# Kernel optimization log

Hardware: AMD Instinct MI355X
Metric: run time of the kernel (lower is better)

The kernel has to match this reference:

```python
import jax, jax.numpy as jnp
import numpy as np

B, C, S, H, W = 8, 64, 64, 128, 128
HID = 32           # max(C//2, 8)
STEPS, DT, OMEGA_MAX = 10, 0.3, 2.0
EPS = 1e-5


def _dw(x, k):
    # depthwise 3x3 conv, NCHW, kernel [C,1,3,3]
    return jax.lax.conv_general_dilated(
        x, k, (1, 1), 'SAME',
        dimension_numbers=('NCHW', 'OIHW', 'NCHW'),
        feature_group_count=x.shape[1])


def _pw(x, w, b=None):
    # pointwise (1x1) conv as einsum, w: [out,in]
    y = jnp.einsum('bihw,oi->bohw', x, w)
    return y if b is None else y + b[None, :, None, None]


def _lrelu(x):
    return jax.nn.leaky_relu(x, 0.2)


def setup_inputs() -> dict:
    key = jax.random.key(0)
    ks = jax.random.split(key, 16)
    d = {
        'force': jax.random.normal(ks[0], (B, C, H, W), jnp.float32),
        'style': jax.random.normal(ks[1], (1, S, 1, 1), jnp.float32),
        'illum_feat': jax.random.normal(ks[2], (B, C, H, W), jnp.float32),
        # HyperEncoder 1x1 convs
        'h_w1': 0.05 * jax.random.normal(ks[3], (HID, C + S), jnp.float32),
        'h_b1': jnp.zeros((HID,), jnp.float32),
        'h_w2': 0.05 * jax.random.normal(ks[4], (HID, HID), jnp.float32),
        'h_b2': jnp.zeros((HID,), jnp.float32),
        'h_w3': 0.05 * jax.random.normal(ks[5], (4 * C, HID), jnp.float32),
        'h_b3': jnp.zeros((4 * C,), jnp.float32),
        # OscillatorCell convs (no bias)
        'dw_k': 0.05 * jax.random.normal(ks[6], (C, 1, 3, 3), jnp.float32),
        'pw_w': 0.05 * jax.random.normal(ks[7], (C, C), jnp.float32),
        # refine: dw3x3 (+bias), pw, lrelu, pw
        'r_dw_k': 0.05 * jax.random.normal(ks[8], (C, 1, 3, 3), jnp.float32),
        'r_dw_b': jnp.zeros((C,), jnp.float32),
        'r_pw1_w': 0.05 * jax.random.normal(ks[9], (C, C), jnp.float32),
        'r_pw1_b': jnp.zeros((C,), jnp.float32),
        'r_pw2_w': 0.05 * jax.random.normal(ks[10], (C, C), jnp.float32),
        'r_pw2_b': jnp.zeros((C,), jnp.float32),
        'layer_scale': 0.01 * jnp.ones((1, C, 1, 1), jnp.float32),
    }
    return d


def reference(force, style, illum_feat,
              h_w1, h_b1, h_w2, h_b2, h_w3, h_b3,
              dw_k, pw_w,
              r_dw_k, r_dw_b, r_pw1_w, r_pw1_b, r_pw2_w, r_pw2_b,
              layer_scale):
    force = force + 0.2 * illum_feat
    b, c, h, w = force.shape

    # HyperEncoder
    style_map = jnp.broadcast_to(style, (b, style.shape[1], h, w))
    u = jnp.concatenate([force, style_map], axis=1)
    u = _lrelu(_pw(u, h_w1, h_b1))
    u = _lrelu(_pw(u, h_w2, h_b2))
    p = _pw(u, h_w3, h_b3)
    wch, zch, gch, bch = jnp.split(p, 4, axis=1)
    omega = jax.nn.sigmoid(wch) * OMEGA_MAX
    zeta = jax.nn.sigmoid(zch)
    gamma = jax.nn.sigmoid(gch) * 2.0
    beta = jnp.tanh(bch)

    # unrolled symplectic-Euler oscillator recurrence
    def step(carry, _):
        x, v = carry
        coupling = _dw(x, dw_k) + _pw(x, pw_w)
        accel = force + coupling - 2.0 * zeta * omega * v - omega ** 2 * x
        v = v + accel * DT
        x = x + v * DT
        return (x, v), None

    x0 = jnp.zeros_like(force)
    (x, v), _ = jax.lax.scan(step, (x0, x0), None, length=STEPS)

    # instance norm (no affine) + style modulation
    fx = force + x
    mu = fx.mean(axis=(2, 3), keepdims=True)
    var = fx.var(axis=(2, 3), keepdims=True)
    out = gamma * ((fx - mu) / jnp.sqrt(var + EPS)) + beta

    # refine branch with layer scale
    r = _dw(out, r_dw_k) + r_dw_b[None, :, None, None]
    r = _lrelu(_pw(r, r_pw1_w, r_pw1_b))
    r = _pw(r, r_pw2_w, r_pw2_b)
    out = out + layer_scale * r
    return (out, x, v)
```

## Files before the change

### kernel.cpp

```cpp
#include <hip/hip_runtime.h>
#include <hip/hip_fp16.h>

#define Hn 128
#define Wn 128
#define HWn 16384
#define Cn 64
#define Bn 8
#define NTOT (Bn*Cn*HWn)
#define NPIX (Bn*HWn)
#define DTc 0.3f
#define EPSc 1e-5f

__device__ __forceinline__ float sigm(float t){ return 1.0f/(1.0f+__expf(-t)); }

__global__ void fuseF0(const float4* __restrict__ force, const float4* __restrict__ illum,
                       __half* __restrict__ F, __half* __restrict__ XA, __half* __restrict__ V)
{
    int i = blockIdx.x * blockDim.x + threadIdx.x;
    float4 f = force[i], il = illum[i];
    float a0 = f.x + 0.2f*il.x, a1 = f.y + 0.2f*il.y;
    float a2 = f.z + 0.2f*il.z, a3 = f.w + 0.2f*il.w;
    uint2 pf, px, pv;
    __half2 h;
    h = __floats2half2_rn(a0, a1);            pf.x = *(unsigned int*)&h;
    h = __floats2half2_rn(a2, a3);            pf.y = *(unsigned int*)&h;
    h = __floats2half2_rn(0.09f*a0, 0.09f*a1); px.x = *(unsigned int*)&h;
    h = __floats2half2_rn(0.09f*a2, 0.09f*a3); px.y = *(unsigned int*)&h;
    h = __floats2half2_rn(0.3f*a0, 0.3f*a1);   pv.x = *(unsigned int*)&h;
    h = __floats2half2_rn(0.3f*a2, 0.3f*a3);   pv.y = *(unsigned int*)&h;
    *reinterpret_cast<uint2*>(F  + 4*(size_t)i) = pf;
    *reinterpret_cast<uint2*>(XA + 4*(size_t)i) = px;
    *reinterpret_cast<uint2*>(V  + 4*(size_t)i) = pv;
}

__global__ void prep(const float* __restrict__ style, const float* __restrict__ w1,
                     const float* __restrict__ b1, const float* __restrict__ pw,
                     const float* __restrict__ pw1, const float* __restrict__ pw2,
                     const float* __restrict__ w3, const float* __restrict__ b3,
                     float* __restrict__ w1T, float* __restrict__ c1,
                     float* __restrict__ pwT, float* __restrict__ pw1T,
                     float* __restrict__ pw2T,
                     __half2* __restrict__ w3abP, __half2* __restrict__ w3gbP,
                     __half2* __restrict__ b3abP, __half2* __restrict__ b3gbP)
{
    int t = threadIdx.x;
    if (t < 32) {
        float s = b1[t];
        for (int k = 0; k < 64; k++) s += w1[t*128 + 64 + k] * style[k];
        c1[t] = s;
    }
    for (int i = t; i < 2048; i += 256) { int c = i >> 5, j = i & 31; w1T[i] = w1[j*128 + c]; }
    for (int i = t; i < 4096; i += 256) {
        int c = i >> 6, k = i & 63;
        pwT[i]  = pw[k*64 + c];
        pw1T[i] = pw1[k*64 + c];
        pw2T[i] = pw2[k*64 + c];
    }
    for (int i = t; i < 2048; i += 256) {
        int j = i >> 5, k = i & 31;
        w3abP[i] = __floats2half2_rn(w3[j*32 + k],         w3[(64 + j)*32 + k]);
        w3gbP[i] = __floats2half2_rn(w3[(128 + j)*32 + k], w3[(192 + j)*32 + k]);
    }
    if (t < 64) {
        b3abP[t] = __floats2half2_rn(b3[t],       b3[64 + t]);
        b3gbP[t] = __floats2half2_rn(b3[128 + t], b3[192 + t]);
    }
}

__global__ __launch_bounds__(256)
void hyperU(const __half* __restrict__ F,
            const float* __restrict__ w1T, const float* __restrict__ c1,
            const float* __restrict__ w2, const float* __restrict__ b2,
            __half* __restrict__ U2)
{
    __shared__ __half fs[64][256];
    int t = threadIdx.x;
    int p0 = blockIdx.x << 8;
    int b  = p0 >> 14;
    int sp0 = p0 & (HWn - 1);
    int tbase = b * Cn * HWn + sp0;

#pragma unroll
    for (int it = 0; it < 8; it++) {
        int f = t + (it << 8);
        int c = f >> 5, u = f & 31;
        uint4 d = *reinterpret_cast<const uint4*>(F + tbase + c*HWn + (u << 3));
        *reinterpret_cast<uint4*>(&fs[c][u << 3]) = d;
    }
    __syncthreads();

    float u1[32];
#pragma unroll
    for (int j = 0; j < 32; j++) u1[j] = c1[j];
#pragma unroll 4
    for (int c = 0; c < 64; c++) {
        float fc = __half2float(fs[c][t]);
        const float* __restrict__ wr = w1T + c*32;
#pragma unroll
        for (int j = 0; j < 32; j++) u1[j] += wr[j] * fc;
    }
#pragma unroll
    for (int j = 0; j < 32; j++) { float v = u1[j]; u1[j] = v > 0.f ? v : 0.2f*v; }

    float u2[32];
#pragma unroll
    for (int i = 0; i < 32; i++) {
        float s = b2[i];
#pragma unroll
        for (int j = 0; j < 32; j++) s += w2[i*32 + j] * u1[j];
        u2[i] = s > 0.f ? s : 0.2f*s;
    }

    uint4* dst = reinterpret_cast<uint4*>(U2 + ((size_t)(p0 + t)) * 32);
#pragma unroll
    for (int q = 0; q < 4; q++) {
        __half2 h0 = __floats2half2_rn(u2[8*q+0], u2[8*q+1]);
        __half2 h1 = __floats2half2_rn(u2[8*q+2], u2[8*q+3]);
        __half2 h2 = __floats2half2_rn(u2[8*q+4], u2[8*q+5]);
        __half2 h3 = __floats2half2_rn(u2[8*q+6], u2[8*q+7]);
        uint4 d;
        d.x = *(unsigned int*)&h0; d.y = *(unsigned int*)&h1;
        d.z = *(unsigned int*)&h2; d.w = *(unsigned int*)&h3;
        dst[q] = d;
    }
}

__global__ __launch_bounds__(256)
void hyperW(const __half* __restrict__ U2,
            const __half2* __restrict__ w3abP, const __half2* __restrict__ w3gbP,
            const __half2* __restrict__ b3abP, const __half2* __restrict__ b3gbP,
            __half2* __restrict__ AB, __half2* __restrict__ GB)
{
    int p = blockIdx.x * blockDim.x + threadIdx.x;
    int b  = p >> 14;
    int sp = p & (HWn - 1);
    int base = b * Cn * HWn + sp;

    __half2 u2b[32];
    const uint4* src = reinterpret_cast<const uint4*>(U2 + (size_t)p * 32);
#pragma unroll
    for (int q = 0; q < 4; q++) {
        uint4 d = src[q];
        __half2 h;
        h = *(__half2*)&d.x; u2b[8*q+0] = __half2half2(__low2half(h)); u2b[8*q+1] = __half2half2(__high2half(h));
        h = *(__half2*)&d.y; u2b[8*q+2] = __half2half2(__low2half(h)); u2b[8*q+3] = __half2half2(__high2half(h));
        h = *(__half2*)&d.z; u2b[8*q+4] = __half2half2(__low2half(h)); u2b[8*q+5] = __half2half2(__high2half(h));
        h = *(__half2*)&d.w; u2b[8*q+6] = __half2half2(__low2half(h)); u2b[8*q+7] = __half2half2(__high2half(h));
    }

    if (blockIdx.y == 0) {
#pragma unroll 2
        for (int j = 0; j < 64; j++) {
            __half2 aab = b3abP[j];
            const __half2* __restrict__ wa = w3abP + j*32;
#pragma unroll
            for (int i = 0; i < 32; i++) aab = __hfma2(wa[i], u2b[i], aab);
            float2 tab = __half22float2(aab);
            float om = 2.0f * sigm(tab.x);
            float ze = sigm(tab.y);
            AB[base + j*HWn] = __floats2half2_rn(2.0f * ze * om, om * om);
        }
    } else {
#pragma unroll 2
        for (int j = 0; j < 64; j++) {
            __half2 agb = b3gbP[j];
            const __half2* __restrict__ wg = w3gbP + j*32;
#pragma unroll
            for (int i = 0; i < 32; i++) agb = __hfma2(wg[i], u2b[i], agb);
            float2 tgb = __half22float2(agb);
            GB[base + j*HWn] = __floats2half2_rn(2.0f * sigm(tgb.x), tanhf(tgb.y));
        }
    }
}

template <bool LAST>
__global__ void osc_step(const __half* __restrict__ Xin, __half* __restrict__ Xout,
                         __half* __restrict__ V, const __half* __restrict__ F,
                         const __half2* __restrict__ AB,
                         const float* __restrict__ dwk, const float* __restrict__ pwT,
                         float* __restrict__ Xf, float* __restrict__ Vf)
{
    int wid  = blockIdx.x;
    int slot = wid >> 3;
    int pc   = ((wid & 7) << 6) + (slot >> 2);
    int c0   = (slot & 3) << 4;
    int p = (pc << 8) + threadIdx.x;
    int b  = p >> 14;
    int sp = p & (HWn - 1);
    int y = sp >> 7, x = sp & 127;
    int base = b * Cn * HWn + sp;

    float acc[16];
#pragma unroll
    for (int k = 0; k < 16; k++) acc[k] = 0.f;
#pragma unroll 4
    for (int c = 0; c < 64; c++) {
        float xc = __half2float(Xin[base + c*HWn]);
        const float* __restrict__ wr = pwT + c*64 + c0;
#pragma unroll
        for (int k = 0; k < 16; k++) acc[k] += wr[k] * xc;
    }

    int   yo[3] = { y > 0 ? -Wn : 0, 0, y < Hn-1 ? Wn : 0 };
    int   xo[3] = { x > 0 ? -1  : 0, 0, x < Wn-1 ? 1  : 0 };
    float my[3] = { y > 0 ? 1.f : 0.f, 1.f, y < Hn-1 ? 1.f : 0.f };
    float mx[3] = { x > 0 ? 1.f : 0.f, 1.f, x < Wn-1 ? 1.f : 0.f };
    float mm[9]; int oo[9];
#pragma unroll
    for (int dy = 0; dy < 3; dy++)
#pragma unroll
        for (int dx = 0; dx < 3; dx++) { mm[dy*3+dx] = my[dy]*mx[dx]; oo[dy*3+dx] = yo[dy]+xo[dx]; }

#pragma unroll
    for (int cc = 0; cc < 16; cc++) {
        int c = c0 + cc;
        int cb = base + c*HWn;
        float tv[9];
#pragma unroll
        for (int t = 0; t < 9; t++) tv[t] = __half2float(Xin[cb + oo[t]]);
        float dws = 0.f;
#pragma unroll
        for (int t = 0; t < 9; t++) dws += (dwk[c*9 + t] * mm[t]) * tv[t];
        float xc = tv[4];
        float2 ab = __half22float2(AB[cb]);
        float vv = __half2float(V[cb]);
        float accel = __half2float(F[cb]) + acc[cc] + dws - ab.x * vv - ab.y * xc;
        vv += accel * DTc;
        float xn = xc + vv * DTc;
        if constexpr (!LAST) {
            V[cb] = __float2half(vv);
            Xout[cb] = __float2half(xn);
        } else {
            Xf[cb] = xn;
            Vf[cb] = vv;
        }
    }
}

__global__ void inorm_stats(const __half* __restrict__ F, const float* __restrict__ X,
                            float* __restrict__ mu, float* __restrict__ rs)
{
    int bc = blockIdx.x;
    int base = bc * HWn;
    const __half2* __restrict__ F2 = (const __half2*)(F + base);
    const float4*  __restrict__ X4 = (const float4*)(X + base);
    float s = 0.f, s2 = 0.f;
    for (int i = threadIdx.x; i < HWn/4; i += blockDim.x) {
        float4 xv = X4[i];
        float2 f0 = __half22float2(F2[2*i]);
        float2 f1 = __half22float2(F2[2*i+1]);
        float v0 = f0.x + xv.x, v1 = f0.y + xv.y, v2 = f1.x + xv.z, v3 = f1.y + xv.w;
        s += (v0 + v1) + (v2 + v3);
        s2 += (v0*v0 + v1*v1) + (v2*v2 + v3*v3);
    }
#pragma unroll
    for (int o = 32; o > 0; o >>= 1) { s += __shfl_down(s, o); s2 += __shfl_down(s2, o); }
    __shared__ float sh[16];
    int w = threadIdx.x >> 6, l = threadIdx.x & 63;
    if (l == 0) { sh[w] = s; sh[8 + w] = s2; }
    __syncthreads();
    if (threadIdx.x == 0) {
        float S = 0.f, S2 = 0.f;
        for (int i = 0; i < 4; i++) { S += sh[i]; S2 += sh[8 + i]; }
        float m = S / (float)HWn;
        float var = S2 / (float)HWn - m*m;
        mu[bc] = m;
        rs[bc] = rsqrtf(var + EPSc);
    }
}

__global__ void modulate(const __half* __restrict__ F, const float4* __restrict__ X4,
                         const uint4* __restrict__ GBu, const float* __restrict__ mu,
                         const float* __restrict__ rs, __half* __restrict__ outp)
{
    int e4 = blockIdx.x * blockDim.x + threadIdx.x;
    int bc = e4 >> 12;
    float m = mu[bc], r = rs[bc];
    uint2 fu = *reinterpret_cast<const uint2*>(F + 4*(size_t)e4);
    float2 f0 = __half22float2(*(__half2*)&fu.x);
    float2 f1 = __half22float2(*(__half2*)&fu.y);
    float4 xv = X4[e4];
    uint4 gb = GBu[e4];
    float2 g0 = __half22float2(*(__half2*)&gb.x);
    float2 g1 = __half22float2(*(__half2*)&gb.y);
    float2 g2 = __half22float2(*(__half2*)&gb.z);
    float2 g3 = __half22float2(*(__half2*)&gb.w);
    float o0 = g0.x * ((f0.x + xv.x - m) * r) + g0.y;
    float o1 = g1.x * ((f0.y + xv.y - m) * r) + g1.y;
    float o2 = g2.x * ((f1.x + xv.z - m) * r) + g2.y;
    float o3 = g3.x * ((f1.y + xv.w - m) * r) + g3.y;
    __half2 h01 = __floats2half2_rn(o0, o1);
    __half2 h23 = __floats2half2_rn(o2, o3);
    uint2 pack; pack.x = *(unsigned int*)&h01; pack.y = *(unsigned int*)&h23;
    *reinterpret_cast<uint2*>(outp + 4*(size_t)e4) = pack;
}

__global__ __launch_bounds__(512)
void refine(const __half* __restrict__ outp,
            const float* __restrict__ rdwk, const float* __restrict__ rdwb,
            const float* __restrict__ pw1T, const float* __restrict__ pb1,
            const float* __restrict__ pw2T, const float* __restrict__ pb2,
            const float* __restrict__ ls, float* __restrict__ out)
{
    __shared__ unsigned int rv2_s[64][64];
    __shared__ unsigned int act2_s[64][64];
    __shared__ __half w1s[64][64];
    __shared__ __half w2s[64][64];
    __shared__ float  dwks[576];
    __shared__ __half2 pb1h[32], pb2h[32];
    __shared__ float  rdwbs[64], lss[64];
    int t = threadIdx.x;
    for (int i = t; i < 4096; i += 512) {
        w1s[i>>6][i&63] = __float2half(pw1T[i]);
        w2s[i>>6][i&63] = __float2half(pw2T[i]);
    }
    for (int i = t; i < 576; i += 512) dwks[i] = rdwk[i];
    if (t < 64) { rdwbs[t]=rdwb[t]; lss[t]=ls[t]; }
    if (t < 32) {
        pb1h[t] = __floats2half2_rn(pb1[2*t], pb1[2*t+1]);
        pb2h[t] = __floats2half2_rn(pb2[2*t], pb2[2*t+1]);
    }

    int l  = t & 63;
    int g  = t >> 6;
    int c0 = g << 3;
    int row = blockIdx.x;
    int b = row >> 7, y = row & 127;
    int base = b * Cn * HWn + y * Wn;
    int px0 = l << 1;

    int   yo[3] = { y > 0 ? -Wn : 0, 0, y < Hn-1 ? Wn : 0 };
    float my[3] = { y > 0 ? 1.f : 0.f, 1.f, y < Hn-1 ? 1.f : 0.f };
    float wl = l > 0  ? 1.f : 0.f;
    float wr = l < 63 ? 1.f : 0.f;
    int loff = l > 0 ? -1 : 0;
    __syncthreads();

#pragma unroll
    for (int cc = 0; cc < 8; cc++) {
        int c = c0 + cc;
        int cb = base + c*HWn + px0;
        float rv0 = rdwbs[c], rv1 = rdwbs[c];
#pragma unroll
        for (int r = 0; r < 3; r++) {
            const __half* __restrict__ rp = outp + cb + yo[r];
            unsigned int cu = *reinterpret_cast<const unsigned int*>(rp);
            float2 ct = __half22float2(*(__half2*)&cu);
            float lf = __half2float(rp[loff]);
            float rt = __half2float(rp[2]);
            float k0 = dwks[c*9 + r*3 + 0] * my[r];
            float k1 = dwks[c*9 + r*3 + 1] * my[r];
            float k2 = dwks[c*9 + r*3 + 2] * my[r];
            rv0 += k0*(wl*lf) + k1*ct.x + k2*ct.y;
            rv1 += k0*ct.x + k1*ct.y + k2*(wr*rt);
        }
        __half2 hv = __floats2half2_rn(rv0, rv1);
        rv2_s[c][l] = *(unsigned int*)&hv;
    }
    __syncthreads();

    __half2 accA[4], accB[4];
#pragma unroll
    for (int q = 0; q < 4; q++) { accA[q] = pb1h[(c0 >> 1) + q]; accB[q] = accA[q]; }
#pragma unroll 8
    for (int c = 0; c < 64; c++) {
        unsigned int rvu = rv2_s[c][l];
        __half2 rvp = *(__half2*)&rvu;
        __half2 r0 = __half2half2(__low2half(rvp));
        __half2 r1 = __half2half2(__high2half(rvp));
        uint4 wq = *reinterpret_cast<const uint4*>(&w1s[c][c0]);
        __half2 w01 = *(__half2*)&wq.x, w23 = *(__half2*)&wq.y;
        __half2 w45 = *(__half2*)&wq.z, w67 = *(__half2*)&wq.w;
        accA[0] = __hfma2(w01, r0, accA[0]); accB[0] = __hfma2(w01, r1, accB[0]);
        accA[1] = __hfma2(w23, r0, accA[1]); accB[1] = __hfma2(w23, r1, accB[1]);
        accA[2] = __hfma2(w45, r0, accA[2]); accB[2] = __hfma2(w45, r1, accB[2]);
        accA[3] = __hfma2(w67, r0, accA[3]); accB[3] = __hfma2(w67, r1, accB[3]);
    }
#pragma unroll
    for (int q = 0; q < 4; q++) {
        float2 a0 = __half22float2(accA[q]);
        float2 a1 = __half22float2(accB[q]);
        float e0 = a0.x > 0.f ? a0.x : 0.2f*a0.x;
        float e1 = a0.y > 0.f ? a0.y : 0.2f*a0.y;
        float e2 = a1.x > 0.f ? a1.x : 0.2f*a1.x;
        float e3 = a1.y > 0.f ? a1.y : 0.2f*a1.y;
        __half2 p0 = __floats2half2_rn(e0, e2);
        __half2 p1 = __floats2half2_rn(e1, e3);
        act2_s[c0 + 2*q][l]     = *(unsigned int*)&p0;
        act2_s[c0 + 2*q + 1][l] = *(unsigned int*)&p1;
    }
    __syncthreads();

#pragma unroll
    for (int q = 0; q < 4; q++) { accA[q] = pb2h[(c0 >> 1) + q]; accB[q] = accA[q]; }
#pragma unroll 8
    for (int j = 0; j < 64; j++) {
        unsigned int au = act2_s[j][l];
        __half2 ap = *(__half2*)&au;
        __half2 a0 = __half2half2(__low2half(ap));
        __half2 a1 = __half2half2(__high2half(ap));
        uint4 wq = *reinterpret_cast<const uint4*>(&w2s[j][c0]);
        __half2 w01 = *(__half2*)&wq.x, w23 = *(__half2*)&wq.y;
        __half2 w45 = *(__half2*)&wq.z, w67 = *(__half2*)&wq.w;
        accA[0] = __hfma2(w01, a0, accA[0]); accB[0] = __hfma2(w01, a1, accB[0]);
        accA[1] = __hfma2(w23, a0, accA[1]); accB[1] = __hfma2(w23, a1, accB[1]);
        accA[2] = __hfma2(w45, a0, accA[2]); accB[2] = __hfma2(w45, a1, accB[2]);
        accA[3] = __hfma2(w67, a0, accA[3]); accB[3] = __hfma2(w67, a1, accB[3]);
    }
#pragma unroll
    for (int q = 0; q < 4; q++) {
        float2 a0 = __half22float2(accA[q]);
        float2 a1 = __half22float2(accB[q]);
        int ca = c0 + 2*q, cb2 = ca + 1;
        int ba = base + ca*HWn + px0;
        int bb = base + cb2*HWn + px0;
        unsigned int oua = *reinterpret_cast<const unsigned int*>(outp + ba);
        unsigned int oub = *reinterpret_cast<const unsigned int*>(outp + bb);
        float2 oa = __half22float2(*(__half2*)&oua);
        float2 ob = __half22float2(*(__half2*)&oub);
        float la = lss[ca], lb = lss[cb2];
        *reinterpret_cast<float2*>(out + ba) = make_float2(oa.x + la*a0.x, oa.y + la*a1.x);
        *reinterpret_cast<float2*>(out + bb) = make_float2(ob.x + lb*a0.y, ob.y + lb*a1.y);
    }
}

extern "C" void kernel_launch(void* const* d_in, const int* in_sizes, int n_in,
                              void* d_out, int out_size, void* d_ws, size_t ws_size,
                              hipStream_t stream)
{
    (void)in_sizes; (void)n_in; (void)out_size; (void)ws_size;
    const float* force   = (const float*)d_in[0];
    const float* style   = (const float*)d_in[1];
    const float* illum   = (const float*)d_in[2];
    const float* h_w1    = (const float*)d_in[3];
    const float* h_b1    = (const float*)d_in[4];
    const float* h_w2    = (const float*)d_in[5];
    const float* h_b2    = (const float*)d_in[6];
    const float* h_w3    = (const float*)d_in[7];
    const float* h_b3    = (const float*)d_in[8];
    const float* dw_k    = (const float*)d_in[9];
    const float* pw_w    = (const float*)d_in[10];
    const float* r_dw_k  = (const float*)d_in[11];
    const float* r_dw_b  = (const float*)d_in[12];
    const float* r_pw1_w = (const float*)d_in[13];
    const float* r_pw1_b = (const float*)d_in[14];
    const float* r_pw2_w = (const float*)d_in[15];
    const float* r_pw2_b = (const float*)d_in[16];
    const float* lscale  = (const float*)d_in[17];

    float* out  = (float*)d_out;
    float* Xf32 = out + (size_t)NTOT;
    float* Vf32 = out + 2*(size_t)NTOT;
    __half2* GB = (__half2*)out;
    __half*  U2h = (__half*)Xf32;

    char* w = (char*)d_ws;
    __half2* AB = (__half2*)w; w += (size_t)NTOT*4;
    __half*  F  = (__half*)w;  w += (size_t)NTOT*2;
    __half*  XA = (__half*)w;  w += (size_t)NTOT*2;
    __half*  XB = (__half*)w;  w += (size_t)NTOT*2;
    __half*  Vh = (__half*)w;  w += (size_t)NTOT*2;
    float* w1T  = (float*)w;
    float* c1   = w1T + 2048;
    float* pwT  = c1 + 32;
    float* pw1T = pwT + 4096;
    float* pw2T = pw1T + 4096;
    float* mu   = pw2T + 4096;
    float* rs   = mu + 512;
    __half2* w3abP = (__half2*)(rs + 512);
    __half2* w3gbP = w3abP + 2048;
    __half2* b3abP = w3gbP + 2048;
    __half2* b3gbP = b3abP + 64;
    __half* outp = (__half*)AB;

    fuseF0<<<NTOT/1024, 256, 0, stream>>>((const float4*)force, (const float4*)illum,
                                          F, XA, Vh);
    prep<<<1, 256, 0, stream>>>(style, h_w1, h_b1, pw_w, r_pw1_w, r_pw2_w, h_w3, h_b3,
                                w1T, c1, pwT, pw1T, pw2T, w3abP, w3gbP, b3abP, b3gbP);
    hyperU<<<NPIX/256, 256, 0, stream>>>(F, w1T, c1, h_w2, h_b2, U2h);
    hyperW<<<dim3(NPIX/256, 2), 256, 0, stream>>>(U2h, w3abP, w3gbP, b3abP, b3gbP, AB, GB);
    for (int s = 1; s <= 8; s++) {
        const __half* xin = (s & 1) ? XA : XB;
        __half*      xout = (s & 1) ? XB : XA;
        osc_step<false><<<2048, 256, 0, stream>>>(xin, xout, Vh, F, AB,
                                                  dw_k, pwT, nullptr, nullptr);
    }
    osc_step<true><<<2048, 256, 0, stream>>>(XA, XB, Vh, F, AB,
                                             dw_k, pwT, Xf32, Vf32);
    inorm_stats<<<Bn*Cn, 256, 0, stream>>>(F, Xf32, mu, rs);
    modulate<<<NTOT/1024, 256, 0, stream>>>(F, (const float4*)Xf32,
                                            (const uint4*)GB, mu, rs, outp);
    refine<<<NPIX/128, 512, 0, stream>>>(outp, r_dw_k, r_dw_b, pw1T, r_pw1_b,
                                         pw2T, r_pw2_b, lscale, out);
}
```

Measured before the change: 482.4 us.

## Fuse force prep into hyperU and compute gamma/beta inside modulation

Removes the separate fuseF0 pass by having hyperU read fp32 force and illum directly, build F in shared memory, and write F, initial X and V from there. The gamma/beta half of the hyper network is no longer precomputed into a full-size GB tensor. Instead the modulation kernel recomputes it from the stored U2 features, which avoids writing and re-reading a large intermediate. U2 moves to its own workspace buffer. The trade-off is extra half-precision FMA work in the modulation stage and scalar, non-vectorized half loads and stores there.

```diff
diff --git a/kernel.cpp b/kernel.cpp
--- a/kernel.cpp
+++ b/kernel.cpp
@@ -13,26 +13,6 @@
 
 __device__ __forceinline__ float sigm(float t){ return 1.0f/(1.0f+__expf(-t)); }
 
-__global__ void fuseF0(const float4* __restrict__ force, const float4* __restrict__ illum,
-                       __half* __restrict__ F, __half* __restrict__ XA, __half* __restrict__ V)
-{
-    int i = blockIdx.x * blockDim.x + threadIdx.x;
-    float4 f = force[i], il = illum[i];
-    float a0 = f.x + 0.2f*il.x, a1 = f.y + 0.2f*il.y;
-    float a2 = f.z + 0.2f*il.z, a3 = f.w + 0.2f*il.w;
-    uint2 pf, px, pv;
-    __half2 h;
-    h = __floats2half2_rn(a0, a1);            pf.x = *(unsigned int*)&h;
-    h = __floats2half2_rn(a2, a3);            pf.y = *(unsigned int*)&h;
-    h = __floats2half2_rn(0.09f*a0, 0.09f*a1); px.x = *(unsigned int*)&h;
-    h = __floats2half2_rn(0.09f*a2, 0.09f*a3); px.y = *(unsigned int*)&h;
-    h = __floats2half2_rn(0.3f*a0, 0.3f*a1);   pv.x = *(unsigned int*)&h;
-    h = __floats2half2_rn(0.3f*a2, 0.3f*a3);   pv.y = *(unsigned int*)&h;
-    *reinterpret_cast<uint2*>(F  + 4*(size_t)i) = pf;
-    *reinterpret_cast<uint2*>(XA + 4*(size_t)i) = px;
-    *reinterpret_cast<uint2*>(V  + 4*(size_t)i) = pv;
-}
-
 __global__ void prep(const float* __restrict__ style, const float* __restrict__ w1,
                      const float* __restrict__ b1, const float* __restrict__ pw,
                      const float* __restrict__ pw1, const float* __restrict__ pw2,
@@ -68,9 +48,10 @@
 }
 
 __global__ __launch_bounds__(256)
-void hyperU(const __half* __restrict__ F,
+void hyperU(const float4* __restrict__ force4, const float4* __restrict__ illum4,
             const float* __restrict__ w1T, const float* __restrict__ c1,
             const float* __restrict__ w2, const float* __restrict__ b2,
+            __half* __restrict__ F, __half* __restrict__ XA, __half* __restrict__ Vh,
             __half* __restrict__ U2)
 {
     __shared__ __half fs[64][256];
@@ -78,16 +59,44 @@
     int p0 = blockIdx.x << 8;
     int b  = p0 >> 14;
     int sp0 = p0 & (HWn - 1);
-    int tbase = b * Cn * HWn + sp0;
+    size_t tbase = (size_t)b * Cn * HWn + sp0;
+    size_t tb4   = tbase >> 2;
+
+#pragma unroll
+    for (int it = 0; it < 16; it++) {
+        int f = t + (it << 8);
+        int c = f >> 6, u = f & 63;
+        size_t gi = tb4 + (size_t)c * (HWn >> 2) + u;
+        float4 fv = force4[gi], iv = illum4[gi];
+        __half2 h0 = __floats2half2_rn(fv.x + 0.2f*iv.x, fv.y + 0.2f*iv.y);
+        __half2 h1 = __floats2half2_rn(fv.z + 0.2f*iv.z, fv.w + 0.2f*iv.w);
+        uint2 pk; pk.x = *(unsigned int*)&h0; pk.y = *(unsigned int*)&h1;
+        *reinterpret_cast<uint2*>(&fs[c][u << 2]) = pk;
+    }
+    __syncthreads();
 
 #pragma unroll
     for (int it = 0; it < 8; it++) {
         int f = t + (it << 8);
         int c = f >> 5, u = f & 31;
-        uint4 d = *reinterpret_cast<const uint4*>(F + tbase + c*HWn + (u << 3));
-        *reinterpret_cast<uint4*>(&fs[c][u << 3]) = d;
-    }
-    __syncthreads();
+        uint4 d = *reinterpret_cast<const uint4*>(&fs[c][u << 3]);
+        size_t gi = tbase + (size_t)c * HWn + (u << 3);
+        *reinterpret_cast<uint4*>(F + gi) = d;
+        uint4 xk, vk;
+        unsigned int* dp = &d.x;
+        unsigned int* xp = &xk.x;
+        unsigned int* vp = &vk.x;
+#pragma unroll
+        for (int q = 0; q < 4; q++) {
+            float2 fv = __half22float2(*(__half2*)&dp[q]);
+            __half2 hx = __floats2half2_rn(0.09f*fv.x, 0.09f*fv.y);
+            __half2 hv = __floats2half2_rn(0.3f*fv.x,  0.3f*fv.y);
+            xp[q] = *(unsigned int*)&hx;
+            vp[q] = *(unsigned int*)&hv;
+        }
+        *reinterpret_cast<uint4*>(XA + gi) = xk;
+        *reinterpret_cast<uint4*>(Vh + gi) = vk;
+    }
 
     float u1[32];
 #pragma unroll
@@ -126,12 +135,12 @@
 }
 
 __global__ __launch_bounds__(256)
-void hyperW(const __half* __restrict__ U2,
-            const __half2* __restrict__ w3abP, const __half2* __restrict__ w3gbP,
-            const __half2* __restrict__ b3abP, const __half2* __restrict__ b3gbP,
-            __half2* __restrict__ AB, __half2* __restrict__ GB)
+void hyperA(const __half* __restrict__ U2,
+            const __half2* __restrict__ w3abP, const __half2* __restrict__ b3abP,
+            __half2* __restrict__ AB)
 {
     int p = blockIdx.x * blockDim.x + threadIdx.x;
+    int j0 = blockIdx.y << 5;
     int b  = p >> 14;
     int sp = p & (HWn - 1);
     int base = b * Cn * HWn + sp;
@@ -148,28 +157,17 @@
         h = *(__half2*)&d.w; u2b[8*q+6] = __half2half2(__low2half(h)); u2b[8*q+7] = __half2half2(__high2half(h));
     }
 
-    if (blockIdx.y == 0) {
 #pragma unroll 2
-        for (int j = 0; j < 64; j++) {
-            __half2 aab = b3abP[j];
-            const __half2* __restrict__ wa = w3abP + j*32;
-#pragma unroll
-            for (int i = 0; i < 32; i++) aab = __hfma2(wa[i], u2b[i], aab);
-            float2 tab = __half22float2(aab);
-            float om = 2.0f * sigm(tab.x);
-            float ze = sigm(tab.y);
-            AB[base + j*HWn] = __floats2half2_rn(2.0f * ze * om, om * om);
-        }
-    } else {
-#pragma unroll 2
-        for (int j = 0; j < 64; j++) {
-            __half2 agb = b3gbP[j];
-            const __half2* __restrict__ wg = w3gbP + j*32;
-#pragma unroll
-            for (int i = 0; i < 32; i++) agb = __hfma2(wg[i], u2b[i], agb);
-            float2 tgb = __half22float2(agb);
-            GB[base + j*HWn] = __floats2half2_rn(2.0f * sigm(tgb.x), tanhf(tgb.y));
-        }
+    for (int jj = 0; jj < 32; jj++) {
+        int j = j0 + jj;
+        __half2 aab = b3abP[j];
+        const __half2* __restrict__ wa = w3abP + j*32;
+#pragma unroll
+        for (int i = 0; i < 32; i++) aab = __hfma2(wa[i], u2b[i], aab);
+        float2 tab = __half22float2(aab);
+        float om = 2.0f * sigm(tab.x);
+        float ze = sigm(tab.y);
+        AB[base + j*HWn] = __floats2half2_rn(2.0f * ze * om, om * om);
     }
 }
 
@@ -269,30 +267,47 @@
     }
 }
 
-__global__ void modulate(const __half* __restrict__ F, const float4* __restrict__ X4,
-                         const uint4* __restrict__ GBu, const float* __restrict__ mu,
-                         const float* __restrict__ rs, __half* __restrict__ outp)
-{
-    int e4 = blockIdx.x * blockDim.x + threadIdx.x;
-    int bc = e4 >> 12;
-    float m = mu[bc], r = rs[bc];
-    uint2 fu = *reinterpret_cast<const uint2*>(F + 4*(size_t)e4);
-    float2 f0 = __half22float2(*(__half2*)&fu.x);
-    float2 f1 = __half22float2(*(__half2*)&fu.y);
-    float4 xv = X4[e4];
-    uint4 gb = GBu[e4];
-    float2 g0 = __half22float2(*(__half2*)&gb.x);
-    float2 g1 = __half22float2(*(__half2*)&gb.y);
-    float2 g2 = __half22float2(*(__half2*)&gb.z);
-    float2 g3 = __half22float2(*(__half2*)&gb.w);
-    float o0 = g0.x * ((f0.x + xv.x - m) * r) + g0.y;
-    float o1 = g1.x * ((f0.y + xv.y - m) * r) + g1.y;
-    float o2 = g2.x * ((f1.x + xv.z - m) * r) + g2.y;
-    float o3 = g3.x * ((f1.y + xv.w - m) * r) + g3.y;
-    __half2 h01 = __floats2half2_rn(o0, o1);
-    __half2 h23 = __floats2half2_rn(o2, o3);
-    uint2 pack; pack.x = *(unsigned int*)&h01; pack.y = *(unsigned int*)&h23;
-    *reinterpret_cast<uint2*>(outp + 4*(size_t)e4) = pack;
+__global__ __launch_bounds__(256)
+void modGB(const __half* __restrict__ U2, const __half* __restrict__ F,
+           const float* __restrict__ X,
+           const __half2* __restrict__ w3gbP, const __half2* __restrict__ b3gbP,
+           const float* __restrict__ mu, const float* __restrict__ rs,
+           __half* __restrict__ outp)
+{
+    int p = blockIdx.x * blockDim.x + threadIdx.x;
+    int j0 = blockIdx.y << 4;
+    int b  = p >> 14;
+    int sp = p & (HWn - 1);
+    int base = b * Cn * HWn + sp;
+
+    __half2 u2b[32];
+    const uint4* src = reinterpret_cast<const uint4*>(U2 + (size_t)p * 32);
+#pragma unroll
+    for (int q = 0; q < 4; q++) {
+        uint4 d = src[q];
+        __half2 h;
+        h = *(__half2*)&d.x; u2b[8*q+0] = __half2half2(__low2half(h)); u2b[8*q+1] = __half2half2(__high2half(h));
+        h = *(__half2*)&d.y; u2b[8*q+2] = __half2half2(__low2half(h)); u2b[8*q+3] = __half2half2(__high2half(h));
+        h = *(__half2*)&d.z; u2b[8*q+4] = __half2half2(__low2half(h)); u2b[8*q+5] = __half2half2(__high2half(h));
+        h = *(__half2*)&d.w; u2b[8*q+6] = __half2half2(__low2half(h)); u2b[8*q+7] = __half2half2(__high2half(h));
+    }
+
+#pragma unroll 2
+    for (int jj = 0; jj < 16; jj++) {
+        int j = j0 + jj;
+        __half2 agb = b3gbP[j];
+        const __half2* __restrict__ wg = w3gbP + j*32;
+#pragma unroll
+        for (int i = 0; i < 32; i++) agb = __hfma2(wg[i], u2b[i], agb);
+        float2 tgb = __half22float2(agb);
+        float gamma = 2.0f * sigm(tgb.x);
+        float beta  = tanhf(tgb.y);
+        int cb = base + j*HWn;
+        int bc = b*64 + j;
+        float fx = __half2float(F[cb]) + X[cb];
+        float o = gamma * ((fx - mu[bc]) * rs[bc]) + beta;
+        outp[cb] = __float2half(o);
+    }
 }
 
 __global__ __launch_bounds__(512)
@@ -451,8 +466,6 @@
     float* out  = (float*)d_out;
     float* Xf32 = out + (size_t)NTOT;
     float* Vf32 = out + 2*(size_t)NTOT;
-    __half2* GB = (__half2*)out;
-    __half*  U2h = (__half*)Xf32;
 
     char* w = (char*)d_ws;
     __half2* AB = (__half2*)w; w += (size_t)NTOT*4;
@@ -460,6 +473,7 @@
     __half*  XA = (__half*)w;  w += (size_t)NTOT*2;
     __half*  XB = (__half*)w;  w += (size_t)NTOT*2;
     __half*  Vh = (__half*)w;  w += (size_t)NTOT*2;
+    __half*  U2h = (__half*)w; w += (size_t)NPIX*32*2;
     float* w1T  = (float*)w;
     float* c1   = w1T + 2048;
     float* pwT  = c1 + 32;
@@ -473,12 +487,11 @@
     __half2* b3gbP = b3abP + 64;
     __half* outp = (__half*)AB;
 
-    fuseF0<<<NTOT/1024, 256, 0, stream>>>((const float4*)force, (const float4*)illum,
-                                          F, XA, Vh);
     prep<<<1, 256, 0, stream>>>(style, h_w1, h_b1, pw_w, r_pw1_w, r_pw2_w, h_w3, h_b3,
                                 w1T, c1, pwT, pw1T, pw2T, w3abP, w3gbP, b3abP, b3gbP);
-    hyperU<<<NPIX/256, 256, 0, stream>>>(F, w1T, c1, h_w2, h_b2, U2h);
-    hyperW<<<dim3(NPIX/256, 2), 256, 0, stream>>>(U2h, w3abP, w3gbP, b3abP, b3gbP, AB, GB);
+    hyperU<<<NPIX/256, 256, 0, stream>>>((const float4*)force, (const float4*)illum,
+                                         w1T, c1, h_w2, h_b2, F, XA, Vh, U2h);
+    hyperA<<<dim3(NPIX/256, 2), 256, 0, stream>>>(U2h, w3abP, b3abP, AB);
     for (int s = 1; s <= 8; s++) {
         const __half* xin = (s & 1) ? XA : XB;
         __half*      xout = (s & 1) ? XB : XA;
@@ -488,8 +501,8 @@
     osc_step<true><<<2048, 256, 0, stream>>>(XA, XB, Vh, F, AB,
                                              dw_k, pwT, Xf32, Vf32);
     inorm_stats<<<Bn*Cn, 256, 0, stream>>>(F, Xf32, mu, rs);
-    modulate<<<NTOT/1024, 256, 0, stream>>>(F, (const float4*)Xf32,
-                                            (const uint4*)GB, mu, rs, outp);
+    modGB<<<dim3(NPIX/256, 4), 256, 0, stream>>>(U2h, F, Xf32, w3gbP, b3gbP,
+                                                 mu, rs, outp);
     refine<<<NPIX/128, 512, 0, stream>>>(outp, r_dw_k, r_dw_b, pw1T, r_pw1_b,
                                          pw2T, r_pw2_b, lscale, out);
 }
```

Result: faster. 453.6 us (-6.0%).
